# Kernel tuning notes

Hardware: AMD Instinct MI355X
Metric: run time of the kernel (lower is better)

Reference implementation:

```python
import jax, jax.numpy as jnp
import numpy as np

N = 12288
C = 1            # n_channels_r
FEAT = 44        # features_dim
RES = 20         # RESIDUE_TYPES_N


def _lin_params(key, fan_in, fan_out):
    k1, k2 = jax.random.split(key)
    bound = 1.0 / np.sqrt(fan_in)
    W = jax.random.uniform(k1, (fan_in, fan_out), minval=-bound, maxval=bound, dtype=jnp.float32)
    b = jax.random.uniform(k2, (fan_out,), minval=-bound, maxval=bound, dtype=jnp.float32)
    return W, b


def setup_inputs() -> dict:
    key = jax.random.key(0)
    ks = jax.random.split(key, 20)
    inp = {
        'one_hot': jax.random.uniform(ks[0], (N, RES), dtype=jnp.float32),
        'features': jax.random.normal(ks[1], (N, FEAT), dtype=jnp.float32),
        'gemme_features': jax.random.normal(ks[2], (N, 1), dtype=jnp.float32),
        'a_res': jax.random.uniform(ks[3], (C, N, N), dtype=jnp.float32),
    }
    # encoder MLP
    inp['We1'], inp['be1'] = _lin_params(ks[4], RES + FEAT, 32)
    inp['We2'], inp['be2'] = _lin_params(ks[5], 32, 64)
    inp['We3'], inp['be3'] = _lin_params(ks[6], 64, 128)
    # graph conv weights: per-relation-channel [C, in, out]
    dims = [(128, 64), (64, 32), (32, 16), (16, 8), (8, 4)]
    for i, (di, do) in enumerate(dims):
        k1, k2 = jax.random.split(ks[7 + i])
        bound = 1.0 / np.sqrt(di)
        inp[f'Wg{i+1}'] = jax.random.uniform(k1, (C, di, do), minval=-bound, maxval=bound, dtype=jnp.float32)
        inp[f'bg{i+1}'] = jax.random.uniform(k2, (do,), minval=-bound, maxval=bound, dtype=jnp.float32)
    # final MLP
    inp['Wf1'], inp['bf1'] = _lin_params(ks[12], 4, 8)
    inp['Wf2'], inp['bf2'] = _lin_params(ks[13], 8, 4)
    inp['Wf3'], inp['bf3'] = _lin_params(ks[14], 4, 1)
    return inp


def _gconv(x, A, W, b):
    # x: [N, in], A: [C, N, N], W: [C, in, out]
    h = jnp.einsum('ni,cio->cno', x, W)          # per-channel linear
    y = jnp.einsum('cmn,cno->mo', A, h) + b      # neighbor aggregation, sum over channels
    return jax.nn.elu(y)


def reference(one_hot, features, gemme_features, a_res,
              We1, be1, We2, be2, We3, be3,
              Wg1, bg1, Wg2, bg2, Wg3, bg3, Wg4, bg4, Wg5, bg5,
              Wf1, bf1, Wf2, bf2, Wf3, bf3):
    x = jnp.concatenate([one_hot, features], axis=1)       # [N, 64]
    x = jax.nn.elu(x @ We1 + be1)                           # dropout = identity (eval)
    x = jax.nn.elu(x @ We2 + be2)
    x = jax.nn.elu(x @ We3 + be3)                           # [N, 128]
    x = _gconv(x, a_res, Wg1, bg1)
    x = _gconv(x, a_res, Wg2, bg2)
    x = _gconv(x, a_res, Wg3, bg3)
    x = _gconv(x, a_res, Wg4, bg4)
    x = _gconv(x, a_res, Wg5, bg5)                          # [N, 4]
    x = jax.nn.elu(x @ Wf1 + bf1)
    x = jax.nn.elu(x @ Wf2 + bf2)
    return jax.nn.sigmoid(x @ Wf3 + bf3)                    # [N, 1]
```

## Files before the change

### kernel.cpp

```cpp
#include <hip/hip_runtime.h>
#include <math.h>

#define NROWS 12288

__device__ __forceinline__ float elu_f(float x) { return x > 0.f ? x : expm1f(x); }

__global__ __launch_bounds__(256) void enc1_kernel(
    const float* __restrict__ oh, const float* __restrict__ ft,
    const float* __restrict__ W, const float* __restrict__ b,
    float* __restrict__ out)
{
    int id = blockIdx.x * 256 + threadIdx.x;
    if (id >= NROWS * 8) return;
    int o4 = id & 7;
    int m  = id >> 3;
    const float4* W4 = reinterpret_cast<const float4*>(W);
    float4 acc = reinterpret_cast<const float4*>(b)[o4];
    const float* ohr = oh + m * 20;
    const float* ftr = ft + m * 44;
#pragma unroll
    for (int i = 0; i < 64; ++i) {
        float x = (i < 20) ? ohr[i] : ftr[i - 20];
        float4 w = W4[i * 8 + o4];
        acc.x = fmaf(x, w.x, acc.x);
        acc.y = fmaf(x, w.y, acc.y);
        acc.z = fmaf(x, w.z, acc.z);
        acc.w = fmaf(x, w.w, acc.w);
    }
    acc.x = elu_f(acc.x); acc.y = elu_f(acc.y);
    acc.z = elu_f(acc.z); acc.w = elu_f(acc.w);
    reinterpret_cast<float4*>(out)[id] = acc;
}

template <int IN, int OUT, bool BIAS, bool ACT_ELU>
__global__ __launch_bounds__(256) void linear4_kernel(
    const float* __restrict__ in, const float* __restrict__ W,
    const float* __restrict__ b, float* __restrict__ out)
{
    constexpr int O4 = OUT / 4;
    int id = blockIdx.x * 256 + threadIdx.x;
    if (id >= NROWS * O4) return;
    int o4 = id % O4;
    int m  = id / O4;
    float4 acc;
    if (BIAS) acc = reinterpret_cast<const float4*>(b)[o4];
    else      acc = make_float4(0.f, 0.f, 0.f, 0.f);
    const float*  ip = in + (size_t)m * IN;
    const float4* W4 = reinterpret_cast<const float4*>(W);
#pragma unroll 8
    for (int i = 0; i < IN; ++i) {
        float  x = ip[i];
        float4 w = W4[i * O4 + o4];
        acc.x = fmaf(x, w.x, acc.x);
        acc.y = fmaf(x, w.y, acc.y);
        acc.z = fmaf(x, w.z, acc.z);
        acc.w = fmaf(x, w.w, acc.w);
    }
    if (ACT_ELU) {
        acc.x = elu_f(acc.x); acc.y = elu_f(acc.y);
        acc.z = elu_f(acc.z); acc.w = elu_f(acc.w);
    }
    reinterpret_cast<float4*>(out)[id] = acc;
}

template <int OUT, int TM, int TN, int SPLIT>
__global__ __launch_bounds__(256) void agg_kernel(
    const float* __restrict__ A, const float* __restrict__ h,
    float* __restrict__ part)
{
    constexpr int BK    = 64;
    constexpr int TCOLS = OUT / TN;
    constexpr int TROWS = 256 / TCOLS;
    constexpr int BM    = TROWS * TM;
    constexpr int MT    = NROWS / BM;
    constexpr int SEG   = NROWS / SPLIT;
    constexpr int HV    = BK * OUT / 4;
    constexpr int HL    = (HV + 255) / 256;

    __shared__ float At[BK][BM + 4];
    __shared__ float Hs[BK][OUT];

    const int tid  = threadIdx.x;
    const int mt   = blockIdx.x % MT;
    const int seg  = blockIdx.x / MT;
    const int m0   = mt * BM;
    const int kb   = seg * SEG;
    const int tcol = tid % TCOLS;
    const int trow = tid / TCOLS;

    const int lr = tid >> 2;
    const int lc = (tid & 3) * 16;

    float acc[TM][TN];
#pragma unroll
    for (int i = 0; i < TM; ++i)
#pragma unroll
        for (int j = 0; j < TN; ++j) acc[i][j] = 0.f;

    for (int k0 = kb; k0 < kb + SEG; k0 += BK) {
        float4 av[BM / 64][4];
#pragma unroll
        for (int p = 0; p < BM / 64; ++p) {
            const float4* src = reinterpret_cast<const float4*>(
                A + (size_t)(m0 + p * 64 + lr) * NROWS + k0 + lc);
            av[p][0] = src[0]; av[p][1] = src[1];
            av[p][2] = src[2]; av[p][3] = src[3];
        }
        float4 hv[HL];
        const float4* hsrc = reinterpret_cast<const float4*>(h + (size_t)k0 * OUT);
#pragma unroll
        for (int i = 0; i < HL; ++i)
            if (HV >= 256 * (i + 1) || i * 256 + tid < HV) hv[i] = hsrc[i * 256 + tid];

        __syncthreads();

#pragma unroll
        for (int p = 0; p < BM / 64; ++p) {
            int r = p * 64 + lr;
#pragma unroll
            for (int v = 0; v < 4; ++v) {
                At[lc + v * 4 + 0][r] = av[p][v].x;
                At[lc + v * 4 + 1][r] = av[p][v].y;
                At[lc + v * 4 + 2][r] = av[p][v].z;
                At[lc + v * 4 + 3][r] = av[p][v].w;
            }
        }
        float4* hdst = reinterpret_cast<float4*>(&Hs[0][0]);
#pragma unroll
        for (int i = 0; i < HL; ++i)
            if (HV >= 256 * (i + 1) || i * 256 + tid < HV) hdst[i * 256 + tid] = hv[i];

        __syncthreads();

#pragma unroll 8
        for (int k = 0; k < BK; ++k) {
            float af[TM];
            if constexpr (TM == 4) {
                float4 t = *reinterpret_cast<const float4*>(&At[k][trow * 4]);
                af[0] = t.x; af[1] = t.y; af[2] = t.z; af[3] = t.w;
            } else if constexpr (TM == 2) {
                float2 t = *reinterpret_cast<const float2*>(&At[k][trow * 2]);
                af[0] = t.x; af[1] = t.y;
            } else {
                af[0] = At[k][trow];
            }
            float hf[TN];
            if constexpr (TN == 8) {
                float4 a = *reinterpret_cast<const float4*>(&Hs[k][tcol * 8]);
                float4 c = *reinterpret_cast<const float4*>(&Hs[k][tcol * 8 + 4]);
                hf[0] = a.x; hf[1] = a.y; hf[2] = a.z; hf[3] = a.w;
                hf[4] = c.x; hf[5] = c.y; hf[6] = c.z; hf[7] = c.w;
            } else if constexpr (TN == 4) {
                float4 a = *reinterpret_cast<const float4*>(&Hs[k][tcol * 4]);
                hf[0] = a.x; hf[1] = a.y; hf[2] = a.z; hf[3] = a.w;
            } else {
                float2 a = *reinterpret_cast<const float2*>(&Hs[k][tcol * 2]);
                hf[0] = a.x; hf[1] = a.y;
            }
#pragma unroll
            for (int i = 0; i < TM; ++i)
#pragma unroll
                for (int j = 0; j < TN; ++j)
                    acc[i][j] = fmaf(af[i], hf[j], acc[i][j]);
        }
    }

    float* pd = part + (size_t)seg * ((size_t)NROWS * OUT);
#pragma unroll
    for (int i = 0; i < TM; ++i) {
        int m = m0 + trow * TM + i;
        float* row = pd + (size_t)m * OUT + tcol * TN;
        if constexpr (TN == 8) {
            *reinterpret_cast<float4*>(row)     = make_float4(acc[i][0], acc[i][1], acc[i][2], acc[i][3]);
            *reinterpret_cast<float4*>(row + 4) = make_float4(acc[i][4], acc[i][5], acc[i][6], acc[i][7]);
        } else if constexpr (TN == 4) {
            *reinterpret_cast<float4*>(row) = make_float4(acc[i][0], acc[i][1], acc[i][2], acc[i][3]);
        } else {
            *reinterpret_cast<float2*>(row) = make_float2(acc[i][0], acc[i][1]);
        }
    }
}

template <int OUT, int SPLIT>
__global__ __launch_bounds__(256) void reduce_kernel(
    const float* __restrict__ part, const float* __restrict__ b,
    float* __restrict__ out)
{
    constexpr int O4 = OUT / 4;
    int id = blockIdx.x * 256 + threadIdx.x;
    if (id >= NROWS * O4) return;
    const float4* p4 = reinterpret_cast<const float4*>(part);
    float4 s = p4[id];
#pragma unroll
    for (int t = 1; t < SPLIT; ++t) {
        float4 v = p4[(size_t)t * (NROWS * O4) + id];
        s.x += v.x; s.y += v.y; s.z += v.z; s.w += v.w;
    }
    float4 bb = reinterpret_cast<const float4*>(b)[id % O4];
    s.x = elu_f(s.x + bb.x); s.y = elu_f(s.y + bb.y);
    s.z = elu_f(s.z + bb.z); s.w = elu_f(s.w + bb.w);
    reinterpret_cast<float4*>(out)[id] = s;
}

__global__ __launch_bounds__(256) void reduce5_final_kernel(
    const float* __restrict__ part, const float* __restrict__ bg,
    const float* __restrict__ Wf1, const float* __restrict__ bf1,
    const float* __restrict__ Wf2, const float* __restrict__ bf2,
    const float* __restrict__ Wf3, const float* __restrict__ bf3,
    float* __restrict__ out)
{
    int m = blockIdx.x * 256 + threadIdx.x;
    if (m >= NROWS) return;
    const float4* p4 = reinterpret_cast<const float4*>(part);
    float4 s = p4[m];
#pragma unroll
    for (int t = 1; t < 16; ++t) {
        float4 v = p4[(size_t)t * NROWS + m];
        s.x += v.x; s.y += v.y; s.z += v.z; s.w += v.w;
    }
    float x0 = elu_f(s.x + bg[0]);
    float x1 = elu_f(s.y + bg[1]);
    float x2 = elu_f(s.z + bg[2]);
    float x3 = elu_f(s.w + bg[3]);

    float t1[8];
#pragma unroll
    for (int o = 0; o < 8; ++o) {
        float a = bf1[o];
        a = fmaf(x0, Wf1[0 * 8 + o], a);
        a = fmaf(x1, Wf1[1 * 8 + o], a);
        a = fmaf(x2, Wf1[2 * 8 + o], a);
        a = fmaf(x3, Wf1[3 * 8 + o], a);
        t1[o] = elu_f(a);
    }
    float t2[4];
#pragma unroll
    for (int o = 0; o < 4; ++o) {
        float a = bf2[o];
#pragma unroll
        for (int i = 0; i < 8; ++i) a = fmaf(t1[i], Wf2[i * 4 + o], a);
        t2[o] = elu_f(a);
    }
    float z = bf3[0];
#pragma unroll
    for (int i = 0; i < 4; ++i) z = fmaf(t2[i], Wf3[i], z);
    out[m] = 1.f / (1.f + expf(-z));
}

static inline dim3 grid_for(int threads) { return dim3((threads + 255) / 256); }

extern "C" void kernel_launch(void* const* d_in, const int* in_sizes, int n_in,
                              void* d_out, int out_size, void* d_ws, size_t ws_size,
                              hipStream_t stream)
{
    (void)in_sizes; (void)n_in; (void)out_size; (void)ws_size;

    const float* one_hot  = (const float*)d_in[0];
    const float* features = (const float*)d_in[1];
    const float* A    = (const float*)d_in[3];
    const float* We1  = (const float*)d_in[4];  const float* be1 = (const float*)d_in[5];
    const float* We2  = (const float*)d_in[6];  const float* be2 = (const float*)d_in[7];
    const float* We3  = (const float*)d_in[8];  const float* be3 = (const float*)d_in[9];
    const float* Wg1  = (const float*)d_in[10]; const float* bg1 = (const float*)d_in[11];
    const float* Wg2  = (const float*)d_in[12]; const float* bg2 = (const float*)d_in[13];
    const float* Wg3  = (const float*)d_in[14]; const float* bg3 = (const float*)d_in[15];
    const float* Wg4  = (const float*)d_in[16]; const float* bg4 = (const float*)d_in[17];
    const float* Wg5  = (const float*)d_in[18]; const float* bg5 = (const float*)d_in[19];
    const float* Wf1  = (const float*)d_in[20]; const float* bf1 = (const float*)d_in[21];
    const float* Wf2  = (const float*)d_in[22]; const float* bf2 = (const float*)d_in[23];
    const float* Wf3  = (const float*)d_in[24]; const float* bf3 = (const float*)d_in[25];
    float* out = (float*)d_out;

    float* bufA = (float*)d_ws;
    float* bufB = bufA + (size_t)NROWS * 128;
    float* hb   = bufB + (size_t)NROWS * 128;
    float* part = hb   + (size_t)NROWS * 64;

    enc1_kernel<<<grid_for(NROWS * 8), 256, 0, stream>>>(one_hot, features, We1, be1, bufB);
    linear4_kernel<32, 64, true, true><<<grid_for(NROWS * 16), 256, 0, stream>>>(bufB, We2, be2, bufA);
    linear4_kernel<64, 128, true, true><<<grid_for(NROWS * 32), 256, 0, stream>>>(bufA, We3, be3, bufB);

    linear4_kernel<128, 64, false, false><<<grid_for(NROWS * 16), 256, 0, stream>>>(bufB, Wg1, nullptr, hb);
    agg_kernel<64, 4, 8, 12><<<dim3(96 * 12), 256, 0, stream>>>(A, hb, part);
    reduce_kernel<64, 12><<<grid_for(NROWS * 16), 256, 0, stream>>>(part, bg1, bufA);

    linear4_kernel<64, 32, false, false><<<grid_for(NROWS * 8), 256, 0, stream>>>(bufA, Wg2, nullptr, hb);
    agg_kernel<32, 2, 8, 16><<<dim3(96 * 16), 256, 0, stream>>>(A, hb, part);
    reduce_kernel<32, 16><<<grid_for(NROWS * 8), 256, 0, stream>>>(part, bg2, bufB);

    linear4_kernel<32, 16, false, false><<<grid_for(NROWS * 4), 256, 0, stream>>>(bufB, Wg3, nullptr, hb);
    agg_kernel<16, 2, 4, 16><<<dim3(96 * 16), 256, 0, stream>>>(A, hb, part);
    reduce_kernel<16, 16><<<grid_for(NROWS * 4), 256, 0, stream>>>(part, bg3, bufA);

    linear4_kernel<16, 8, false, false><<<grid_for(NROWS * 2), 256, 0, stream>>>(bufA, Wg4, nullptr, hb);
    agg_kernel<8, 1, 4, 16><<<dim3(96 * 16), 256, 0, stream>>>(A, hb, part);
    reduce_kernel<8, 16><<<grid_for(NROWS * 2), 256, 0, stream>>>(part, bg4, bufB);

    linear4_kernel<8, 4, false, false><<<grid_for(NROWS), 256, 0, stream>>>(bufB, Wg5, nullptr, hb);
    agg_kernel<4, 1, 2, 16><<<dim3(96 * 16), 256, 0, stream>>>(A, hb, part);
    reduce5_final_kernel<<<grid_for(NROWS), 256, 0, stream>>>(part, bg5, Wf1, bf1, Wf2, bf2, Wf3, bf3, out);
}
```

Baseline: 1.640 ms.

## Restructure aggregation kernel with register prefetch, XOR-swizzled LDS and larger tiles

Rewrites the adjacency aggregation GEMM so every layer uses a fixed 256-row by 32-k tile and a 16-way k-split. The next A/h tile is loaded into registers while the current tile is computed from shared memory, overlapping global loads with FMAs. The padded transposed shared-memory tile is replaced by an XOR-swizzled layout, and a 3-blocks-per-CU launch bound is added. This trades shorter global row segments per thread and more register pressure for fewer, larger blocks and hidden load latency on the dominant bandwidth-bound A reads.

```diff
diff --git a/kernel.cpp b/kernel.cpp
--- a/kernel.cpp
+++ b/kernel.cpp
@@ -63,99 +63,106 @@
     reinterpret_cast<float4*>(out)[id] = acc;
 }
 
-template <int OUT, int TM, int TN, int SPLIT>
-__global__ __launch_bounds__(256) void agg_kernel(
+template <int OUT, int TM, int TN>
+__global__ __launch_bounds__(256, 3) void agg_kernel(
     const float* __restrict__ A, const float* __restrict__ h,
     float* __restrict__ part)
 {
-    constexpr int BK    = 64;
+    constexpr int BK = 32, BM = 256, SPLIT = 16;
     constexpr int TCOLS = OUT / TN;
     constexpr int TROWS = 256 / TCOLS;
-    constexpr int BM    = TROWS * TM;
-    constexpr int MT    = NROWS / BM;
-    constexpr int SEG   = NROWS / SPLIT;
-    constexpr int HV    = BK * OUT / 4;
-    constexpr int HL    = (HV + 255) / 256;
-
-    __shared__ float At[BK][BM + 4];
+    static_assert(TROWS * TM == BM, "tile mismatch");
+    constexpr int MT  = NROWS / BM;
+    constexpr int SEG = NROWS / SPLIT;
+    constexpr int NT  = SEG / BK;
+    constexpr int HV  = BK * OUT / 4;
+    constexpr int HL  = (HV + 255) / 256;
+
+    __shared__ float At[BK][BM];
     __shared__ float Hs[BK][OUT];
 
-    const int tid  = threadIdx.x;
-    const int mt   = blockIdx.x % MT;
-    const int seg  = blockIdx.x / MT;
-    const int m0   = mt * BM;
-    const int kb   = seg * SEG;
+    const int tid = threadIdx.x;
+    const int mt  = blockIdx.x % MT;
+    const int seg = blockIdx.x / MT;
+    const int m0  = mt * BM;
+    const int kb  = seg * SEG;
+
+    const int r0 = tid >> 3;
+    const int c4 = tid & 7;
     const int tcol = tid % TCOLS;
     const int trow = tid / TCOLS;
 
-    const int lr = tid >> 2;
-    const int lc = (tid & 3) * 16;
-
-    float acc[TM][TN];
-#pragma unroll
-    for (int i = 0; i < TM; ++i)
-#pragma unroll
-        for (int j = 0; j < TN; ++j) acc[i][j] = 0.f;
-
-    for (int k0 = kb; k0 < kb + SEG; k0 += BK) {
-        float4 av[BM / 64][4];
-#pragma unroll
-        for (int p = 0; p < BM / 64; ++p) {
-            const float4* src = reinterpret_cast<const float4*>(
-                A + (size_t)(m0 + p * 64 + lr) * NROWS + k0 + lc);
-            av[p][0] = src[0]; av[p][1] = src[1];
-            av[p][2] = src[2]; av[p][3] = src[3];
-        }
-        float4 hv[HL];
+    const float* Abase = A + (size_t)(m0 + r0) * NROWS + c4 * 4;
+
+    float4 av[8];
+    float4 hv[HL];
+
+    auto load_tile = [&](int k0) {
+#pragma unroll
+        for (int p = 0; p < 8; ++p)
+            av[p] = *reinterpret_cast<const float4*>(Abase + (size_t)(p * 32) * NROWS + k0);
         const float4* hsrc = reinterpret_cast<const float4*>(h + (size_t)k0 * OUT);
 #pragma unroll
         for (int i = 0; i < HL; ++i)
             if (HV >= 256 * (i + 1) || i * 256 + tid < HV) hv[i] = hsrc[i * 256 + tid];
-
+    };
+
+    float acc[TM][TN];
+#pragma unroll
+    for (int i = 0; i < TM; ++i)
+#pragma unroll
+        for (int j = 0; j < TN; ++j) acc[i][j] = 0.f;
+
+    load_tile(kb);
+
+    for (int t = 0; t < NT; ++t) {
         __syncthreads();
-
-#pragma unroll
-        for (int p = 0; p < BM / 64; ++p) {
-            int r = p * 64 + lr;
-#pragma unroll
-            for (int v = 0; v < 4; ++v) {
-                At[lc + v * 4 + 0][r] = av[p][v].x;
-                At[lc + v * 4 + 1][r] = av[p][v].y;
-                At[lc + v * 4 + 2][r] = av[p][v].z;
-                At[lc + v * 4 + 3][r] = av[p][v].w;
-            }
+        const int sw = c4 * 4;
+#pragma unroll
+        for (int p = 0; p < 8; ++p) {
+            const int md = (r0 + p * 32) ^ sw;
+            At[sw + 0][md] = av[p].x;
+            At[sw + 1][md] = av[p].y;
+            At[sw + 2][md] = av[p].z;
+            At[sw + 3][md] = av[p].w;
         }
         float4* hdst = reinterpret_cast<float4*>(&Hs[0][0]);
 #pragma unroll
         for (int i = 0; i < HL; ++i)
             if (HV >= 256 * (i + 1) || i * 256 + tid < HV) hdst[i * 256 + tid] = hv[i];
-
         __syncthreads();
 
-#pragma unroll 8
-        for (int k = 0; k < BK; ++k) {
+        if (t + 1 < NT) load_tile(kb + (t + 1) * BK);
+
+#pragma unroll
+        for (int kk = 0; kk < BK; ++kk) {
+            const int s24 = kk & 24, s4 = kk & 4;
             float af[TM];
-            if constexpr (TM == 4) {
-                float4 t = *reinterpret_cast<const float4*>(&At[k][trow * 4]);
-                af[0] = t.x; af[1] = t.y; af[2] = t.z; af[3] = t.w;
-            } else if constexpr (TM == 2) {
-                float2 t = *reinterpret_cast<const float2*>(&At[k][trow * 2]);
-                af[0] = t.x; af[1] = t.y;
+            if constexpr (TM == 8) {
+                const int base8 = (trow * 8) ^ s24;
+                float4 a0 = *reinterpret_cast<const float4*>(&At[kk][base8 + s4]);
+                float4 a1 = *reinterpret_cast<const float4*>(&At[kk][base8 + (s4 ^ 4)]);
+                af[0] = a0.x; af[1] = a0.y; af[2] = a0.z; af[3] = a0.w;
+                af[4] = a1.x; af[5] = a1.y; af[6] = a1.z; af[7] = a1.w;
             } else {
-                af[0] = At[k][trow];
+                const int b4 = (trow * 4) ^ (s24 | s4);
+                float4 a0 = *reinterpret_cast<const float4*>(&At[kk][b4]);
+                af[0] = a0.x; af[1] = a0.y; af[2] = a0.z; af[3] = a0.w;
             }
             float hf[TN];
             if constexpr (TN == 8) {
-                float4 a = *reinterpret_cast<const float4*>(&Hs[k][tcol * 8]);
-                float4 c = *reinterpret_cast<const float4*>(&Hs[k][tcol * 8 + 4]);
-                hf[0] = a.x; hf[1] = a.y; hf[2] = a.z; hf[3] = a.w;
-                hf[4] = c.x; hf[5] = c.y; hf[6] = c.z; hf[7] = c.w;
+                float4 b0 = *reinterpret_cast<const float4*>(&Hs[kk][tcol * 8]);
+                float4 b1 = *reinterpret_cast<const float4*>(&Hs[kk][tcol * 8 + 4]);
+                hf[0] = b0.x; hf[1] = b0.y; hf[2] = b0.z; hf[3] = b0.w;
+                hf[4] = b1.x; hf[5] = b1.y; hf[6] = b1.z; hf[7] = b1.w;
             } else if constexpr (TN == 4) {
-                float4 a = *reinterpret_cast<const float4*>(&Hs[k][tcol * 4]);
-                hf[0] = a.x; hf[1] = a.y; hf[2] = a.z; hf[3] = a.w;
+                float4 b0 = *reinterpret_cast<const float4*>(&Hs[kk][tcol * 4]);
+                hf[0] = b0.x; hf[1] = b0.y; hf[2] = b0.z; hf[3] = b0.w;
+            } else if constexpr (TN == 2) {
+                float2 b0 = *reinterpret_cast<const float2*>(&Hs[kk][tcol * 2]);
+                hf[0] = b0.x; hf[1] = b0.y;
             } else {
-                float2 a = *reinterpret_cast<const float2*>(&Hs[k][tcol * 2]);
-                hf[0] = a.x; hf[1] = a.y;
+                hf[0] = Hs[kk][tcol];
             }
 #pragma unroll
             for (int i = 0; i < TM; ++i)
@@ -168,15 +175,17 @@
     float* pd = part + (size_t)seg * ((size_t)NROWS * OUT);
 #pragma unroll
     for (int i = 0; i < TM; ++i) {
-        int m = m0 + trow * TM + i;
+        const int m = m0 + trow * TM + i;
         float* row = pd + (size_t)m * OUT + tcol * TN;
         if constexpr (TN == 8) {
             *reinterpret_cast<float4*>(row)     = make_float4(acc[i][0], acc[i][1], acc[i][2], acc[i][3]);
             *reinterpret_cast<float4*>(row + 4) = make_float4(acc[i][4], acc[i][5], acc[i][6], acc[i][7]);
         } else if constexpr (TN == 4) {
             *reinterpret_cast<float4*>(row) = make_float4(acc[i][0], acc[i][1], acc[i][2], acc[i][3]);
+        } else if constexpr (TN == 2) {
+            *reinterpret_cast<float2*>(row) = make_float2(acc[i][0], acc[i][1]);
         } else {
-            *reinterpret_cast<float2*>(row) = make_float2(acc[i][0], acc[i][1]);
+            row[0] = acc[i][0];
         }
     }
 }
@@ -276,27 +285,29 @@
     float* hb   = bufB + (size_t)NROWS * 128;
     float* part = hb   + (size_t)NROWS * 64;
 
+    const dim3 agrid(48 * 16);
+
     enc1_kernel<<<grid_for(NROWS * 8), 256, 0, stream>>>(one_hot, features, We1, be1, bufB);
     linear4_kernel<32, 64, true, true><<<grid_for(NROWS * 16), 256, 0, stream>>>(bufB, We2, be2, bufA);
     linear4_kernel<64, 128, true, true><<<grid_for(NROWS * 32), 256, 0, stream>>>(bufA, We3, be3, bufB);
 
     linear4_kernel<128, 64, false, false><<<grid_for(NROWS * 16), 256, 0, stream>>>(bufB, Wg1, nullptr, hb);
-    agg_kernel<64, 4, 8, 12><<<dim3(96 * 12), 256, 0, stream>>>(A, hb, part);
-    reduce_kernel<64, 12><<<grid_for(NROWS * 16), 256, 0, stream>>>(part, bg1, bufA);
+    agg_kernel<64, 8, 8><<<agrid, 256, 0, stream>>>(A, hb, part);
+    reduce_kernel<64, 16><<<grid_for(NROWS * 16), 256, 0, stream>>>(part, bg1, bufA);
 
     linear4_kernel<64, 32, false, false><<<grid_for(NROWS * 8), 256, 0, stream>>>(bufA, Wg2, nullptr, hb);
-    agg_kernel<32, 2, 8, 16><<<dim3(96 * 16), 256, 0, stream>>>(A, hb, part);
+    agg_kernel<32, 8, 4><<<agrid, 256, 0, stream>>>(A, hb, part);
     reduce_kernel<32, 16><<<grid_for(NROWS * 8), 256, 0, stream>>>(part, bg2, bufB);
 
     linear4_kernel<32, 16, false, false><<<grid_for(NROWS * 4), 256, 0, stream>>>(bufB, Wg3, nullptr, hb);
-    agg_kernel<16, 2, 4, 16><<<dim3(96 * 16), 256, 0, stream>>>(A, hb, part);
+    agg_kernel<16, 8, 2><<<agrid, 256, 0, stream>>>(A, hb, part);
     reduce_kernel<16, 16><<<grid_for(NROWS * 4), 256, 0, stream>>>(part, bg3, bufA);
 
     linear4_kernel<16, 8, false, false><<<grid_for(NROWS * 2), 256, 0, stream>>>(bufA, Wg4, nullptr, hb);
-    agg_kernel<8, 1, 4, 16><<<dim3(96 * 16), 256, 0, stream>>>(A, hb, part);
+    agg_kernel<8, 8, 1><<<agrid, 256, 0, stream>>>(A, hb, part);
     reduce_kernel<8, 16><<<grid_for(NROWS * 2), 256, 0, stream>>>(part, bg4, bufB);
 
     linear4_kernel<8, 4, false, false><<<grid_for(NROWS), 256, 0, stream>>>(bufB, Wg5, nullptr, hb);
-    agg_kernel<4, 1, 2, 16><<<dim3(96 * 16), 256, 0, stream>>>(A, hb, part);
+    agg_kernel<4, 4, 1><<<agrid, 256, 0, stream>>>(A, hb, part);
     reduce5_final_kernel<<<grid_for(NROWS), 256, 0, stream>>>(part, bg5, Wf1, bf1, Wf2, bf2, Wf3, bf3, out);
 }
```

Result: slower. 2.022 ms (+23.3%).
